# Kernel optimization log

Hardware: AMD Instinct MI355X
Metric: run time of the kernel (lower is better)

## Reference

```python
import jax, jax.numpy as jnp
import numpy as np
from jax import lax

B, N, F, H = 8, 2048, 256, 128
RATIO = 0.5
NUM_LAYERS = 2
K = int(N * RATIO) + 1  # num coarse nodes per layer


def setup_inputs() -> dict:
    key = jax.random.key(0)
    ks = jax.random.split(key, 8)
    x = jax.random.normal(ks[0], (B, N, F), dtype=jnp.float32)
    a = jax.random.uniform(ks[1], (B, N, N), dtype=jnp.float32)
    adj = (a < 0.005).astype(jnp.float32)
    adj = jnp.maximum(adj, adj.transpose(0, 2, 1))
    mask = jnp.ones((B, N), dtype=jnp.float32)
    W1 = jax.random.normal(ks[2], (F, H), dtype=jnp.float32) * (1.0 / np.sqrt(F))
    b1 = jnp.zeros((H,), dtype=jnp.float32)
    Watt = jax.random.normal(ks[3], (H, 1), dtype=jnp.float32) * (1.0 / np.sqrt(H))
    batt = jnp.zeros((1,), dtype=jnp.float32)
    W2 = jax.random.normal(ks[4], (H, F), dtype=jnp.float32) * (1.0 / np.sqrt(H))
    b2 = jnp.zeros((F,), dtype=jnp.float32)
    return {"x": x, "adj": adj, "mask": mask, "W1": W1, "b1": b1,
            "Watt": Watt, "batt": batt, "W2": W2, "b2": b2}


def dense_gcn(x, adj, W, b, mask):
    # PyG DenseGCNConv with add_loop=True: set diag to 1, sym-normalize, propagate
    n = adj.shape[-1]
    eye = jnp.eye(n, dtype=adj.dtype)
    a = adj * (1.0 - eye) + eye
    d = jnp.maximum(a.sum(-1), 1.0) ** -0.5            # [B,N]
    an = d[..., :, None] * a * d[..., None, :]
    out = jnp.einsum('bnm,bmh->bnh', an, x @ W) + b
    return out * mask[..., None]


def normalize_batch_adj(adj):
    n = adj.shape[-1]
    A = adj + jnp.eye(n, dtype=adj.dtype)
    d = jnp.maximum(A.sum(-1), 1.0) ** -0.5
    newA = d[..., :, None] * A * d[..., None, :]
    row_nonzero = (adj.sum(-1) > 0).astype(adj.dtype)  # zero out isolated-node rows
    return row_nonzero[..., None] * newA


def coarsen_block(x, adj, Watt, batt, k):
    norm_adj = normalize_batch_adj(adj)
    # attention GCN -> squared -> sigmoid
    alpha = jnp.einsum('bnm,bm->bn', norm_adj, (x @ Watt + batt).squeeze(-1))
    alpha = jax.nn.sigmoid(alpha ** 2)                 # [B,N]
    topv, topi = lax.top_k(alpha, k)
    cut = topv[:, -1]                                  # k-th largest value per graph
    cut_alpha = jax.nn.relu(alpha + 1e-7 - cut[:, None])
    S = norm_adj * cut_alpha[:, None, :]               # scale columns
    S = S / jnp.maximum(jnp.abs(S).sum(-1, keepdims=True), 1e-12)  # L1 row-normalize
    x2 = jnp.einsum('bnm,bnf->bmf', S, x)              # S^T x
    A2 = jnp.einsum('bnm,bnk,bkl->bml', S, adj, S)     # S^T A S
    A2 = jnp.floor(A2 * 1e4) / 1e4                     # 4-digit floor quantization
    return x2, A2, S, topi


def reference(x, adj, mask, W1, b1, Watt, batt, W2, b2):
    x1 = jax.nn.relu(dense_gcn(x, adj, W1, b1, mask))  # [B,N,H]
    coarse_x, new_adj = x1, adj
    for _ in range(NUM_LAYERS):
        coarse_x, new_adj, S, topi = coarsen_block(coarse_x, new_adj, Watt, batt, K)
    x2 = dense_gcn(coarse_x, new_adj, W2, b2, mask)    # [B,N,F]
    # JumpingKnowledge 'cat' of pooled readouts
    return jnp.concatenate([x1.mean(axis=1), x2.mean(axis=1)], axis=-1)  # [B,H+F]
```

## Files before the change

### kernel.cpp

```cpp
#include <hip/hip_runtime.h>
#include <math.h>

#define NN 2048
#define NB 8
#define FF 256
#define HH 128
#define KSEL 1025
#define NROWS (NB*NN)
#define MPAD 1152
#define MC (MPAD*NB)
#define LMAX 64
#define MI 6
#define RSTRIDE 2052
#define ZIDX 2048
#define LP 72

typedef unsigned short ushort_t;
typedef __attribute__((ext_vector_type(8))) short short8;
typedef __attribute__((ext_vector_type(4))) float f32x4;

__device__ inline ushort_t f2bf(float f) {
  unsigned u = __float_as_uint(f);
  unsigned r = (u + 0x7FFFu + ((u >> 16) & 1u)) >> 16;
  return (ushort_t)r;
}
__device__ inline float bf2f(ushort_t u) {
  unsigned x = ((unsigned)u) << 16;
  return __uint_as_float(x);
}

#define GLDS16(g, l) __builtin_amdgcn_global_load_lds( \
    (const __attribute__((address_space(1))) unsigned int*)(g), \
    (__attribute__((address_space(3))) unsigned int*)(l), 16, 0, 0)

__global__ __launch_bounds__(256) void rowstats_k(const float* __restrict__ A,
                                                  ushort_t* __restrict__ klist,
                                                  int* __restrict__ kcnt,
                                                  float* __restrict__ diag,
                                                  float* __restrict__ dgcn,
                                                  float* __restrict__ dnorm,
                                                  float* __restrict__ rz, int R) {
  int gw = (blockIdx.x * 256 + threadIdx.x) >> 6;
  int lane = threadIdx.x & 63;
  int b = gw / R, i = gw - b * R;
  const float4* row = (const float4*)(A + (long long)gw * R);
  int R4 = R >> 2;
  float s = 0.f;
  ushort_t* lst = klist ? (klist + (long long)gw * LMAX) : (ushort_t*)0;
  int base = 0;
  for (int j = lane; j < R4; j += 64) {
    float4 v = row[j];
    s += v.x + v.y + v.z + v.w;
    if (klist) {
      int c0 = (v.x != 0.f), c1 = (v.y != 0.f), c2 = (v.z != 0.f), c3 = (v.w != 0.f);
      int c = c0 + c1 + c2 + c3;
      int pref = c;
#pragma unroll
      for (int off = 1; off < 64; off <<= 1) {
        int t = __shfl_up(pref, off);
        if (lane >= off) pref += t;
      }
      int tot = __shfl(pref, 63);
      int p = base + pref - c;
      int col = j * 4;
      if (c0) { if (p < LMAX) lst[p] = (ushort_t)col;       p++; }
      if (c1) { if (p < LMAX) lst[p] = (ushort_t)(col + 1); p++; }
      if (c2) { if (p < LMAX) lst[p] = (ushort_t)(col + 2); p++; }
      if (c3) { if (p < LMAX) lst[p] = (ushort_t)(col + 3); p++; }
      base += tot;
    }
  }
  for (int off = 32; off > 0; off >>= 1) s += __shfl_down(s, off);
  if (lane == 0) {
    float dg = A[(long long)gw * R + i];
    diag[gw] = dg;
    dgcn[gw]  = rsqrtf(fmaxf(s - dg + 1.f, 1.f));
    dnorm[gw] = rsqrtf(fmaxf(s + 1.f, 1.f));
    rz[gw]    = s > 0.f ? 1.f : 0.f;
    if (kcnt) kcnt[gw] = base < LMAX ? base : LMAX;
  }
}

__global__ __launch_bounds__(256) void rowstatsw_k(const float* __restrict__ A,
                                                   const float* __restrict__ X,
                                                   const float* __restrict__ Watt,
                                                   const float* __restrict__ batt,
                                                   float* __restrict__ dnorm,
                                                   float* __restrict__ rz,
                                                   float* __restrict__ w, int R) {
  int gw = (blockIdx.x * 256 + threadIdx.x) >> 6;
  int lane = threadIdx.x & 63;
  int b = gw / R;
  const float4* row = (const float4*)(A + (long long)gw * R);
  int R4 = R >> 2;
  float s = 0.f;
  for (int j = lane; j < R4; j += 64) {
    float4 v = row[j];
    s += v.x + v.y + v.z + v.w;
  }
  for (int off = 32; off > 0; off >>= 1) s += __shfl_xor(s, off);
  float dn = rsqrtf(fmaxf(s + 1.f, 1.f));
  const float* xr = X + (long long)gw * HH;
  float t = xr[lane] * Watt[lane] + xr[lane + 64] * Watt[lane + 64];
  for (int off = 32; off > 0; off >>= 1) t += __shfl_down(t, off);
  if (lane == 0) {
    dnorm[gw] = dn;
    rz[gw]    = s > 0.f ? 1.f : 0.f;
    w[gw] = dn * (t + batt[0]);
  }
}

__global__ __launch_bounds__(256) void spmm1e_k(const ushort_t* __restrict__ klist,
                                                const int* __restrict__ kcnt,
                                                const float* __restrict__ dgcn,
                                                const float* __restrict__ diag,
                                                const float* __restrict__ b1,
                                                const float* __restrict__ mask,
                                                const float* __restrict__ Watt,
                                                const float* __restrict__ batt,
                                                const float* __restrict__ dnorm,
                                                const float* __restrict__ xw,
                                                float* __restrict__ xa,
                                                float* __restrict__ w) {
  int bid = blockIdx.x;
  int sw = (bid & 7) * ((int)gridDim.x >> 3) + (bid >> 3);
  int gw = (sw * 256 + threadIdx.x) >> 6;
  int lane = threadIdx.x & 63;
  int b = gw >> 11;
  int cnt = kcnt[gw];
  const ushort_t* kl = klist + (long long)gw * LMAX;
  int myk = (lane < cnt) ? (int)kl[lane] : 0;
  float myd = dgcn[b * NN + myk];
  float s0 = 0.f, s1 = 0.f;
  for (int t = 0; t < cnt; t++) {
    int k = __shfl(myk, t);
    float d = __shfl(myd, t);
    const float* xr = xw + ((long long)b * NN + k) * HH;
    s0 += d * xr[lane];
    s1 += d * xr[lane + 64];
  }
  long long o = (long long)gw * HH;
  float d = dgcn[gw];
  float dgv = diag[gw];
  float mv = mask[gw];
  float xw0 = xw[o + lane], xw1v = xw[o + lane + 64];
  float t0 = d * (s0 + (1.f - dgv) * d * xw0) + b1[lane];
  float t1 = d * (s1 + (1.f - dgv) * d * xw1v) + b1[lane + 64];
  t0 *= mv; t1 *= mv;
  float x0 = fmaxf(t0, 0.f), x1 = fmaxf(t1, 0.f);
  xa[o + lane] = x0;
  xa[o + lane + 64] = x1;
  float t = x0 * Watt[lane] + x1 * Watt[lane + 64];
  for (int off = 32; off > 0; off >>= 1) t += __shfl_down(t, off);
  if (lane == 0) w[gw] = dnorm[gw] * (t + batt[0]);
}

__global__ __launch_bounds__(256) void spmm2_k(const ushort_t* __restrict__ klistC,
                                               const int* __restrict__ kcntC,
                                               const float* __restrict__ scalev,
                                               const float* __restrict__ cwk,
                                               const float* __restrict__ xa,
                                               float* __restrict__ x2c) {
  int bid = blockIdx.x;
  int sw = (bid & 7) * ((int)gridDim.x >> 3) + (bid >> 3);
  int gw = (sw * 256 + threadIdx.x) >> 6;
  int lane = threadIdx.x & 63;
  int b = gw / MPAD;
  int cnt = kcntC[gw];
  const ushort_t* kl = klistC + (long long)gw * LP;
  int c64 = cnt < 64 ? cnt : 64;
  int myk = (lane < c64) ? (int)kl[lane] : 0;
  float myc = scalev[b * NN + myk];
  float s0 = 0.f, s1 = 0.f;
  for (int t = 0; t < c64; t++) {
    int k = __shfl(myk, t);
    float c = __shfl(myc, t);
    const float* xr = xa + ((long long)b * NN + k) * HH;
    s0 += c * xr[lane];
    s1 += c * xr[lane + 64];
  }
  if (cnt > 64) {
    int k = kl[64];
    float c = scalev[b * NN + k];
    const float* xr = xa + ((long long)b * NN + k) * HH;
    s0 += c * xr[lane];
    s1 += c * xr[lane + 64];
  }
  float cw = cwk[gw];
  long long o = (long long)gw * HH;
  x2c[o + lane] = cw * s0;
  x2c[o + lane + 64] = cw * s1;
}

__global__ __launch_bounds__(256) void alphaL_k(const ushort_t* __restrict__ klist,
                                                const int* __restrict__ kcnt,
                                                const float* __restrict__ w,
                                                const float* __restrict__ dnorm,
                                                const float* __restrict__ rz,
                                                float* __restrict__ alpha) {
  int gw = (blockIdx.x * 256 + threadIdx.x) >> 6;
  int lane = threadIdx.x & 63;
  int b = gw >> 11, i = gw & (NN - 1);
  int cnt = kcnt[gw];
  float s = 0.f;
  if (lane < cnt) s = w[(long long)b * NN + klist[(long long)gw * LMAX + lane]];
  for (int off = 32; off > 0; off >>= 1) s += __shfl_down(s, off);
  if (lane == 0) {
    float aa = rz[gw] * dnorm[gw] * (s + w[(long long)b * NN + i]);
    aa = aa * aa;
    alpha[(long long)b * NN + i] = 1.f / (1.f + expf(-aa));
  }
}

__global__ __launch_bounds__(256) void alpha_k(const float* __restrict__ A,
                                               const float* __restrict__ w,
                                               const float* __restrict__ dnorm,
                                               const float* __restrict__ rz,
                                               float* __restrict__ alpha, int R) {
  int gw = (blockIdx.x * 256 + threadIdx.x) >> 6;
  int lane = threadIdx.x & 63;
  int b = gw / R, i = gw - b * R;
  const float4* row = (const float4*)(A + (long long)gw * R);
  const float4* wb4 = (const float4*)(w + (long long)b * R);
  int R4 = R >> 2;
  float s = 0.f;
  for (int j = lane; j < R4; j += 64) {
    float4 a = row[j], ww = wb4[j];
    s += a.x * ww.x + a.y * ww.y + a.z * ww.z + a.w * ww.w;
  }
  for (int off = 32; off > 0; off >>= 1) s += __shfl_down(s, off);
  if (lane == 0) {
    float aa = rz[gw] * dnorm[gw] * (s + w[(long long)b * R + i]);
    aa = aa * aa;
    alpha[(long long)b * NN + i] = 1.f / (1.f + expf(-aa));
  }
}

__global__ __launch_bounds__(1024) void topkeep_k(const float* __restrict__ alpha,
                                                  const float* __restrict__ dnorm,
                                                  const float* __restrict__ rz,
                                                  float* __restrict__ colw,
                                                  int* __restrict__ keepidx) {
  __shared__ unsigned vals[NN];
  __shared__ int hist[256];
  __shared__ int wsum[32];
  __shared__ unsigned selp_s;
  __shared__ int selr_s;
  int b = blockIdx.x, t = threadIdx.x;
  vals[t] = __float_as_uint(alpha[b * NN + t]);
  vals[t + 1024] = __float_as_uint(alpha[b * NN + t + 1024]);
  if (t == 0) { selp_s = 0u; selr_s = KSEL; }
  __syncthreads();
  for (int shift = 24; shift >= 0; shift -= 8) {
    if (t < 256) hist[t] = 0;
    __syncthreads();
    unsigned pre = selp_s; int rank = selr_s;
    unsigned hm = (shift == 24) ? 0u : (0xFFFFFFFFu << (shift + 8));
    for (int e = t; e < NN; e += 1024) {
      unsigned v = vals[e];
      if ((v & hm) == (pre & hm)) atomicAdd(&hist[(v >> shift) & 255], 1);
    }
    __syncthreads();
    for (int off2 = 1; off2 < 256; off2 <<= 1) {
      int v = 0;
      if (t < 256 - off2) v = hist[t + off2];
      __syncthreads();
      if (t < 256 - off2) hist[t] += v;
      __syncthreads();
    }
    if (t < 256) {
      int cge = hist[t];
      int cgt = (t == 255) ? 0 : hist[t + 1];
      if (cge >= rank && cgt < rank) {
        selp_s = pre | ((unsigned)t << shift);
        selr_s = rank - cgt;
      }
    }
    __syncthreads();
  }
  float cu = __uint_as_float(selp_s);
  float a0 = __uint_as_float(vals[t]);
  float a1 = __uint_as_float(vals[t + 1024]);
  float c0 = dnorm[b * NN + t]        * fmaxf(a0 + 1e-7f - cu, 0.f);
  float c1 = dnorm[b * NN + t + 1024] * fmaxf(a1 + 1e-7f - cu, 0.f);
  colw[b * NN + t] = c0;
  colw[b * NN + t + 1024] = c1;
  int f0 = (c0 != 0.f && rz[b * NN + t]        != 0.f) ? 1 : 0;
  int f1 = (c1 != 0.f && rz[b * NN + t + 1024] != 0.f) ? 1 : 0;
  int lane = t & 63, wid = t >> 6;
  unsigned long long m0 = __ballot(f0);
  unsigned long long m1 = __ballot(f1);
  if (lane == 0) { wsum[wid] = __popcll(m0); wsum[16 + wid] = __popcll(m1); }
  __syncthreads();
  if (t == 0) { int run = 0; for (int i2 = 0; i2 < 32; i2++) { int v = wsum[i2]; wsum[i2] = run; run += v; } }
  __syncthreads();
  unsigned long long lm = (1ull << lane) - 1ull;
  int p0 = wsum[wid] + __popcll(m0 & lm);
  int p1 = wsum[16 + wid] + __popcll(m1 & lm);
  if (t < MPAD) keepidx[b * MPAD + t] = -1;
  if (t + 1024 < MPAD) keepidx[b * MPAD + t + 1024] = -1;
  __syncthreads();
  if (f0 && p0 < MPAD) keepidx[b * MPAD + p0] = t;
  if (f1 && p1 < MPAD) keepidx[b * MPAD + p1] = t + 1024;
}

__global__ __launch_bounds__(1024) void topcolw_k(const float* __restrict__ alpha,
                                                  const float* __restrict__ dnorm,
                                                  float* __restrict__ colw) {
  __shared__ unsigned vals[NN];
  __shared__ int hist[256];
  __shared__ unsigned selp_s;
  __shared__ int selr_s;
  int b = blockIdx.x, t = threadIdx.x;
  vals[t] = __float_as_uint(alpha[b * NN + t]);
  vals[t + 1024] = (t + 1024 >= MPAD) ? __float_as_uint(0.5f)
                                      : __float_as_uint(alpha[b * NN + t + 1024]);
  if (t == 0) { selp_s = 0u; selr_s = KSEL; }
  __syncthreads();
  for (int shift = 24; shift >= 0; shift -= 8) {
    if (t < 256) hist[t] = 0;
    __syncthreads();
    unsigned pre = selp_s; int rank = selr_s;
    unsigned hm = (shift == 24) ? 0u : (0xFFFFFFFFu << (shift + 8));
    for (int e = t; e < NN; e += 1024) {
      unsigned v = vals[e];
      if ((v & hm) == (pre & hm)) atomicAdd(&hist[(v >> shift) & 255], 1);
    }
    __syncthreads();
    for (int off2 = 1; off2 < 256; off2 <<= 1) {
      int v = 0;
      if (t < 256 - off2) v = hist[t + off2];
      __syncthreads();
      if (t < 256 - off2) hist[t] += v;
      __syncthreads();
    }
    if (t < 256) {
      int cge = hist[t];
      int cgt = (t == 255) ? 0 : hist[t + 1];
      if (cge >= rank && cgt < rank) {
        selp_s = pre | ((unsigned)t << shift);
        selr_s = rank - cgt;
      }
    }
    __syncthreads();
  }
  float cu = __uint_as_float(selp_s);
  for (int ii = t; ii < MPAD; ii += 1024) {
    float c = fmaxf(__uint_as_float(vals[ii]) + 1e-7f - cu, 0.f);
    colw[b * MPAD + ii] = dnorm[b * MPAD + ii] * c;
  }
}

__global__ __launch_bounds__(256) void scaleL_k(const ushort_t* __restrict__ klist,
                                                const int* __restrict__ kcnt,
                                                const float* __restrict__ colw,
                                                const float* __restrict__ dnorm,
                                                const float* __restrict__ rz,
                                                float* __restrict__ scale) {
  int gw = (blockIdx.x * 256 + threadIdx.x) >> 6;
  int lane = threadIdx.x & 63;
  int b = gw >> 11, i = gw & (NN - 1);
  int cnt = kcnt[gw];
  float s = 0.f;
  if (lane < cnt) s = colw[(long long)b * NN + klist[(long long)gw * LMAX + lane]];
  for (int off = 32; off > 0; off >>= 1) s += __shfl_down(s, off);
  if (lane == 0) {
    float rsum = rz[gw] * dnorm[gw] * (s + colw[(long long)b * NN + i]);
    scale[gw] = rz[gw] * dnorm[gw] / fmaxf(rsum, 1e-12f);
  }
}

__global__ __launch_bounds__(256) void scale_k(const float* __restrict__ A,
                                               const float* __restrict__ colw,
                                               const float* __restrict__ dnorm,
                                               const float* __restrict__ rz,
                                               float* __restrict__ scale, int R) {
  int gw = (blockIdx.x * 256 + threadIdx.x) >> 6;
  int lane = threadIdx.x & 63;
  int b = gw / R, i = gw - b * R;
  const float4* row = (const float4*)(A + (long long)gw * R);
  const float4* cw4 = (const float4*)(colw + (long long)b * R);
  int R4 = R >> 2;
  float s = 0.f;
  for (int j = lane; j < R4; j += 64) {
    float4 a = row[j], c = cw4[j];
    s += a.x * c.x + a.y * c.y + a.z * c.z + a.w * c.w;
  }
  for (int off = 32; off > 0; off >>= 1) s += __shfl_down(s, off);
  if (lane == 0) {
    float rsum = rz[gw] * dnorm[gw] * (s + colw[(long long)b * R + i]);
    scale[gw] = rz[gw] * dnorm[gw] / fmaxf(rsum, 1e-12f);
  }
}

__global__ __launch_bounds__(256) void packlist_k(const ushort_t* __restrict__ klist,
                                                  const int* __restrict__ kcnt,
                                                  const int* __restrict__ keepidx,
                                                  const float* __restrict__ colw,
                                                  ushort_t* __restrict__ klistC,
                                                  int* __restrict__ kcntC,
                                                  float* __restrict__ cwk) {
  int g = blockIdx.x * 256 + threadIdx.x;
  int b = g / MPAD;
  int rj = keepidx[g];
  ushort_t* dst = klistC + (long long)g * LP;
  int cnt = 0;
  if (rj >= 0) {
    long long gr = (long long)b * NN + rj;
    int c = kcnt[gr];
    const ushort_t* src = klist + gr * LMAX;
    for (int t = 0; t < c; t++) dst[t] = src[t];
    dst[c] = (ushort_t)rj;
    cnt = c + 1;
  }
  kcntC[g] = cnt;
  cwk[g] = (rj >= 0) ? colw[b * NN + rj] : 0.f;
  int pad = (cnt + 7) & ~7;
  for (int t = cnt; t < pad; t++) dst[t] = (ushort_t)ZIDX;
}

__global__ void zero_k(float* __restrict__ p) {
  p[blockIdx.x * 256 + threadIdx.x] = 0.f;
}

__global__ __launch_bounds__(256) void sparseA2f_k(const ushort_t* __restrict__ klist,
                                                   const int* __restrict__ kcnt,
                                                   const int* __restrict__ keepidx,
                                                   const float* __restrict__ scalev,
                                                   const ushort_t* __restrict__ klistC,
                                                   const int* __restrict__ kcntC,
                                                   const float* __restrict__ cwk,
                                                   float* __restrict__ A2cF,
                                                   ushort_t* __restrict__ A2cH,
                                                   ushort_t* __restrict__ A2cL) {
  __shared__ float Rs[3 * RSTRIDE * 2];
  int i0 = blockIdx.x * MI;
  int b = i0 / MPAD, im0 = i0 - b * MPAD;
  int tid = threadIdx.x;
  int wid = tid >> 6, lane = tid & 63;
  const float* sb = scalev + (long long)b * NN;

  float4 z4 = make_float4(0.f, 0.f, 0.f, 0.f);
  for (int n = tid * 4; n < 3 * RSTRIDE * 2; n += 1024) *(float4*)&Rs[n] = z4;
  __syncthreads();

  for (int rr = wid; rr < MI; rr += 4) {
    int r = keepidx[i0 + rr];
    if (r < 0) continue;
    int p = rr >> 1, q = rr & 1;
    float* plane = Rs + p * RSTRIDE * 2;
    long long gr = (long long)b * NN + r;
    int cr = kcnt[gr];
    int myk = (lane < cr) ? (int)klist[gr * LMAX + lane] : r;
    float mycoef = sb[myk];
    int mycnt = kcnt[(long long)b * NN + myk];
    for (int i = 0; i < cr; i++) {
      int k = __shfl(myk, i);
      float coef = __shfl(mycoef, i);
      int ck = __shfl(mycnt, i);
      if (lane < ck) {
        int n = (int)klist[((long long)b * NN + k) * LMAX + lane];
        plane[n * 2 + q] += coef;
      }
    }
    float coef = sb[r];
    if (lane < cr) plane[myk * 2 + q] += coef;
  }
  __syncthreads();

  for (int c = tid; c < NN; c += 256) {
    float sc = sb[c];
#pragma unroll
    for (int p = 0; p < 3; p++) {
      float2* e = (float2*)&Rs[(p * RSTRIDE + c) * 2];
      float2 v = *e; v.x *= sc; v.y *= sc; *e = v;
    }
  }
  __syncthreads();

  float cwi[MI];
#pragma unroll
  for (int r = 0; r < MI; r++) cwi[r] = cwk[i0 + r];
  long long ob = (long long)b * MPAD * MPAD + (long long)im0 * MPAD;
  for (int j = tid; j < MPAD; j += 256) {
    int cnt = kcntC[b * MPAD + j];
    const ushort_t* kl = klistC + (long long)(b * MPAD + j) * LP;
    float sx0 = 0.f, sy0 = 0.f, sx1 = 0.f, sy1 = 0.f, sx2 = 0.f, sy2 = 0.f;
    int rounds = (cnt + 7) >> 3;
    for (int t0 = 0; t0 < rounds; t0++) {
      uint4 kv = *(const uint4*)(kl + t0 * 8);
      const ushort_t* kp = (const ushort_t*)&kv;
#pragma unroll
      for (int t = 0; t < 8; t++) {
        int c = kp[t];
        float2 v0 = *(const float2*)&Rs[(0 * RSTRIDE + c) * 2];
        float2 v1 = *(const float2*)&Rs[(1 * RSTRIDE + c) * 2];
        float2 v2 = *(const float2*)&Rs[(2 * RSTRIDE + c) * 2];
        sx0 += v0.x; sy0 += v0.y;
        sx1 += v1.x; sy1 += v1.y;
        sx2 += v2.x; sy2 += v2.y;
      }
    }
    float sv[MI] = {sx0, sy0, sx1, sy1, sx2, sy2};
    float cwj = cwk[b * MPAD + j];
#pragma unroll
    for (int r = 0; r < MI; r++) {
      float vq = floorf(cwi[r] * cwj * sv[r] * 10000.f) / 10000.f;
      ushort_t h = f2bf(vq);
      long long o = ob + (long long)r * MPAD + j;
      A2cF[o] = vq;
      A2cH[o] = h;
      A2cL[o] = f2bf(vq - bf2f(h));
    }
  }
}

__global__ void writeS2c_k(const float* __restrict__ A2c, const float* __restrict__ scale,
                           const float* __restrict__ colw,
                           ushort_t* __restrict__ Sh, ushort_t* __restrict__ Sl) {
  int g = blockIdx.x * 256 + threadIdx.x;
  int bl = g / (MPAD / 4);
  int k = (g - bl * (MPAD / 4)) * 4;
  int b = bl / MPAD, l = bl - b * MPAD;
  long long o = (long long)bl * MPAD + k;
  float cw = colw[b * MPAD + l];
  float4 sc = *(const float4*)(scale + b * MPAD + k);
  float4 av = *(const float4*)(A2c + o);
  float v0 = sc.x * (av.x + (float)(k     == l)) * cw;
  float v1 = sc.y * (av.y + (float)(k + 1 == l)) * cw;
  float v2 = sc.z * (av.z + (float)(k + 2 == l)) * cw;
  float v3 = sc.w * (av.w + (float)(k + 3 == l)) * cw;
  ushort_t h0 = f2bf(v0), h1 = f2bf(v1), h2 = f2bf(v2), h3 = f2bf(v3);
  *(uint2*)&Sh[o] = make_uint2((unsigned)h0 | ((unsigned)h1 << 16),
                               (unsigned)h2 | ((unsigned)h3 << 16));
  ushort_t l0 = f2bf(v0 - bf2f(h0)), l1 = f2bf(v1 - bf2f(h1));
  ushort_t l2 = f2bf(v2 - bf2f(h2)), l3 = f2bf(v3 - bf2f(h3));
  *(uint2*)&Sl[o] = make_uint2((unsigned)l0 | ((unsigned)l1 << 16),
                               (unsigned)l2 | ((unsigned)l3 << 16));
}

template<int SA, int SB, int EPI, int BN>
__global__ __launch_bounds__(256) void mgemm_k(
    const ushort_t* __restrict__ Ah, const ushort_t* __restrict__ Al,
    const ushort_t* __restrict__ Bh, const ushort_t* __restrict__ Bl,
    float* __restrict__ Co, ushort_t* __restrict__ Toh, ushort_t* __restrict__ Tol,
    float* __restrict__ rs, float* __restrict__ dgv,
    int M, int Ncol, int K, long long sA, long long sB, long long sC,
    int gx, int ks, long long sPart) {
  constexpr int NJ = BN / 32;
  __shared__ ushort_t Ahs[128 * 32];
  __shared__ ushort_t Bhs[BN * 32];
  __shared__ ushort_t Als[SA ? 128 * 32 : 64];
  __shared__ ushort_t Bls[SB ? BN * 32 : 64];

  int tid = threadIdx.x;
  int id = blockIdx.x;
  long long bz = id & 7;
  int rest = id >> 3;
  int kslice = rest % ks;
  int t0 = rest / ks;
  int tn = t0 % gx, tm = t0 / gx;
  int n0 = tn * BN, m0 = tm * 128;
  const ushort_t* Ahb = Ah + bz * sA;
  const ushort_t* Alb = SA ? (Al + bz * sA) : Ah;
  const ushort_t* Bhb = Bh + bz * sB;
  const ushort_t* Blb = SB ? (Bl + bz * sB) : Bh;

  int sr = tid >> 2;
  int sc = (tid & 3) * 8;
  int lane = tid & 63, w = tid >> 6;
  int wm = (w >> 1) * 64, wn = (w & 1) * (BN / 2);
  int fr = lane & 15;
  int fo = (lane >> 4) * 8;
  int q = lane >> 4;

  f32x4 acc[4][NJ];
  f32x4 zz = {0.f, 0.f, 0.f, 0.f};
#pragma unroll
  for (int i = 0; i < 4; i++)
#pragma unroll
    for (int j = 0; j < NJ; j++) acc[i][j] = zz;

  int Kpc = K / ks;
  int kbeg = kslice * Kpc;
  for (int k0 = kbeg; k0 < kbeg + Kpc; k0 += 32) {
    __syncthreads();
#pragma unroll
    for (int r = 0; r < 128; r += 64) {
      GLDS16(Ahb + (long long)(m0 + sr + r) * K + k0 + sc, &Ahs[(r + sr) * 32 + sc]);
      if constexpr (SA) {
        GLDS16(Alb + (long long)(m0 + sr + r) * K + k0 + sc, &Als[(r + sr) * 32 + sc]);
      }
    }
#pragma unroll
    for (int r = 0; r < BN; r += 64) {
      GLDS16(Bhb + (long long)(n0 + sr + r) * K + k0 + sc, &Bhs[(r + sr) * 32 + sc]);
      if constexpr (SB) {
        GLDS16(Blb + (long long)(n0 + sr + r) * K + k0 + sc, &Bls[(r + sr) * 32 + sc]);
      }
    }
    __syncthreads();

    short8 ah[4], al[4], bh[NJ], bl[NJ];
#pragma unroll
    for (int i = 0; i < 4; i++) {
      ah[i] = *(const short8*)&Ahs[(wm + i * 16 + fr) * 32 + fo];
      if constexpr (SA) al[i] = *(const short8*)&Als[(wm + i * 16 + fr) * 32 + fo];
    }
#pragma unroll
    for (int j = 0; j < NJ; j++) {
      bh[j] = *(const short8*)&Bhs[(wn + j * 16 + fr) * 32 + fo];
      if constexpr (SB) bl[j] = *(const short8*)&Bls[(wn + j * 16 + fr) * 32 + fo];
    }
#pragma unroll
    for (int i = 0; i < 4; i++)
#pragma unroll
      for (int j = 0; j < NJ; j++) {
        acc[i][j] = __builtin_amdgcn_mfma_f32_16x16x32_bf16(ah[i], bh[j], acc[i][j], 0, 0, 0);
        if constexpr (SB)
          acc[i][j] = __builtin_amdgcn_mfma_f32_16x16x32_bf16(ah[i], bl[j], acc[i][j], 0, 0, 0);
        if constexpr (SA)
          acc[i][j] = __builtin_amdgcn_mfma_f32_16x16x32_bf16(al[i], bh[j], acc[i][j], 0, 0, 0);
      }
  }

  if constexpr (EPI == 6) {
#pragma unroll
    for (int i = 0; i < 4; i++)
#pragma unroll
      for (int r = 0; r < 4; r++) {
        int row = m0 + wm + i * 16 + q * 4 + r;
        long long rb = bz * sC + (long long)row * Ncol;
        float rp = 0.f;
#pragma unroll
        for (int j = 0; j < NJ; j++) {
          int col = n0 + wn + j * 16 + fr;
          float vq = floorf(acc[i][j][r] * 10000.f) / 10000.f;
          Co[rb + col] = vq;
          rp += vq;
          if (col == row) dgv[bz * MPAD + row] = vq;
        }
#pragma unroll
        for (int o2 = 8; o2 > 0; o2 >>= 1) rp += __shfl_down(rp, o2, 16);
        if (fr == 0) atomicAdd(&rs[bz * MPAD + row], rp);
      }
  } else {
#pragma unroll
    for (int i = 0; i < 4; i++)
#pragma unroll
      for (int j = 0; j < NJ; j++)
#pragma unroll
        for (int r = 0; r < 4; r++) {
          float v = acc[i][j][r];
          int row = m0 + wm + i * 16 + q * 4 + r;
          int col = n0 + wn + j * 16 + fr;
          long long idx = bz * sC + (long long)row * Ncol + col;
          if constexpr (EPI == 0) {
            Co[kslice * sPart + idx] = v;
          } else {
            ushort_t h = f2bf(v);
            Toh[idx] = h;
            Tol[idx] = f2bf(v - bf2f(h));
          }
        }
  }
}

__global__ void dstat_k(const float* __restrict__ rs, const float* __restrict__ dgv,
                        float* __restrict__ dgcn) {
  int g = blockIdx.x * 256 + threadIdx.x;
  dgcn[g] = rsqrtf(fmaxf(rs[g] - dgv[g] + 1.f, 1.f));
}

__global__ __launch_bounds__(256) void wfin_k(const float* __restrict__ A3,
                                              const float* __restrict__ dgcn,
                                              const float* __restrict__ diag,
                                              float* __restrict__ wv) {
  int gw = (blockIdx.x * 256 + threadIdx.x) >> 6;
  int lane = threadIdx.x & 63;
  int b = gw / MPAD;
  const float4* row = (const float4*)(A3 + (long long)gw * MPAD);
  const float4* d4 = (const float4*)(dgcn + (long long)b * MPAD);
  float s = 0.f;
  for (int j = lane; j < MPAD / 4; j += 64) {
    float4 a = row[j], d = d4[j];
    s += a.x * d.x + a.y * d.y + a.z * d.z + a.w * d.w;
  }
  for (int off = 32; off > 0; off >>= 1) s += __shfl_down(s, off);
  if (lane == 0) {
    float dl = dgcn[gw];
    wv[gw] = dl * (s - dl * diag[gw] + dl);
  }
}

__global__ __launch_bounds__(256) void zfin_k(const float* __restrict__ A2c,
                                              const float* __restrict__ scalev,
                                              const float* __restrict__ colwv,
                                              const float* __restrict__ wv,
                                              float* __restrict__ zv) {
  int gw = (blockIdx.x * 256 + threadIdx.x) >> 6;
  int lane = threadIdx.x & 63;
  int b = gw / MPAD;
  const float4* row = (const float4*)(A2c + (long long)gw * MPAD);
  const float4* c4 = (const float4*)(colwv + (long long)b * MPAD);
  const float4* w4 = (const float4*)(wv + (long long)b * MPAD);
  float s = 0.f;
  for (int j = lane; j < MPAD / 4; j += 64) {
    float4 a = row[j], c = c4[j], w = w4[j];
    s += a.x * c.x * w.x + a.y * c.y * w.y + a.z * c.z * w.z + a.w * c.w * w.w;
  }
  for (int off = 32; off > 0; off >>= 1) s += __shfl_down(s, off);
  if (lane == 0) {
    zv[gw] = scalev[gw] * (s + colwv[gw] * wv[gw]);
  }
}

__global__ void zx_k(const float* __restrict__ zv, const float* __restrict__ x2c,
                     float* __restrict__ part) {
  int b = blockIdx.y, c = blockIdx.x, h = threadIdx.x;
  const float* p = x2c + ((long long)(b * MPAD + c * 128)) * HH + h;
  const float* zp = zv + b * MPAD + c * 128;
  float s = 0.f;
  for (int r = 0; r < 128; r++) s += zp[r] * p[(long long)r * HH];
  part[(b * 9 + c) * HH + h] = s;
}

__global__ __launch_bounds__(256) void fout2_k(const float* __restrict__ part,
                                               const float* __restrict__ W2,
                                               const float* __restrict__ b2,
                                               float* __restrict__ out) {
  __shared__ float wx3[HH];
  int b = blockIdx.x, f = threadIdx.x;
  if (f < HH) {
    float s = 0.f;
    for (int c = 0; c < 9; c++) s += part[(b * 9 + c) * HH + f];
    wx3[f] = s;
  }
  __syncthreads();
  float s = 0.f;
  for (int h = 0; h < HH; h++) s += wx3[h] * W2[h * FF + f];
  out[b * (HH + FF) + HH + f] = b2[f] + s * (1.f / NN);
}

__global__ void pmean_k(const float* __restrict__ X, float* __restrict__ part,
                        int Nn, int Fd, int rpc) {
  int b = blockIdx.y, c = blockIdx.x, f = threadIdx.x;
  const float* p = X + ((long long)b * Nn + (long long)c * rpc) * Fd + f;
  float s = 0.f;
  for (int r = 0; r < rpc; r++) s += p[(long long)r * Fd];
  part[((long long)b * gridDim.x + c) * Fd + f] = s;
}

__global__ void fmean_k(const float* __restrict__ part, int nch, int Fd, float corr,
                        const float* __restrict__ bias, float* __restrict__ out, int outoff) {
  int b = blockIdx.x, f = threadIdx.x;
  float s = 0.f;
  for (int c = 0; c < nch; c++) s += part[((long long)b * nch + c) * Fd + f];
  float cv = bias ? corr * bias[f] : 0.f;
  out[b * (HH + FF) + outoff + f] = s * (1.f / NN) + cv;
}

__global__ __launch_bounds__(256) void gemm_k(const float* __restrict__ A, const float* __restrict__ B,
                                              float* __restrict__ C,
                                              int M, int Nw, int Kk,
                                              long long sA, long long sB, long long sC) {
  __shared__ float As[16][128];
  __shared__ float Bs[16][128];
  int tid = threadIdx.x;
  int n0 = blockIdx.x * 128, m0 = blockIdx.y * 128;
  int bz = blockIdx.z;
  const float* Ab = A + (long long)bz * sA;
  const float* Bb = B + (long long)bz * sB;
  float* Cb = C + (long long)bz * sC;
  float acc[8][8];
#pragma unroll
  for (int i = 0; i < 8; i++)
#pragma unroll
    for (int j = 0; j < 8; j++) acc[i][j] = 0.f;
  int tx = tid & 15, ty = tid >> 4;

  for (int k0 = 0; k0 < Kk; k0 += 16) {
    {
      int r = tid >> 2, c = (tid & 3) << 2;
#pragma unroll
      for (int rr = 0; rr < 2; rr++) {
        int rrow = r + rr * 64;
        float4 v = *(const float4*)(Ab + (long long)(m0 + rrow) * Kk + k0 + c);
        As[c + 0][rrow] = v.x; As[c + 1][rrow] = v.y;
        As[c + 2][rrow] = v.z; As[c + 3][rrow] = v.w;
      }
    }
    {
      int kk = tid >> 5, cc = (tid & 31) << 2;
#pragma unroll
      for (int k2 = 0; k2 < 2; k2++) {
        float4 v = *(const float4*)(Bb + (long long)(k0 + kk + k2 * 8) * Nw + n0 + cc);
        *(float4*)&Bs[kk + k2 * 8][cc] = v;
      }
    }
    __syncthreads();
#pragma unroll
    for (int kk = 0; kk < 16; kk++) {
      float a[8], bb[8];
      *(float4*)&a[0]  = *(float4*)&As[kk][ty * 8];
      *(float4*)&a[4]  = *(float4*)&As[kk][ty * 8 + 4];
      *(float4*)&bb[0] = *(float4*)&Bs[kk][tx * 8];
      *(float4*)&bb[4] = *(float4*)&Bs[kk][tx * 8 + 4];
#pragma unroll
      for (int i = 0; i < 8; i++)
#pragma unroll
        for (int j = 0; j < 8; j++) acc[i][j] += a[i] * bb[j];
    }
    __syncthreads();
  }
#pragma unroll
  for (int i = 0; i < 8; i++) {
    float* cp = Cb + (long long)(m0 + ty * 8 + i) * Nw + n0 + tx * 8;
    *(float4*)cp = *(float4*)&acc[i][0];
    *(float4*)(cp + 4) = *(float4*)&acc[i][4];
  }
}

extern "C" void kernel_launch(void* const* d_in, const int* in_sizes, int n_in,
                              void* d_out, int out_size, void* d_ws, size_t ws_size,
                              hipStream_t stream) {
  const float* x    = (const float*)d_in[0];
  const float* adj  = (const float*)d_in[1];
  const float* mask = (const float*)d_in[2];
  const float* W1   = (const float*)d_in[3];
  const float* b1   = (const float*)d_in[4];
  const float* Watt = (const float*)d_in[5];
  const float* batt = (const float*)d_in[6];
  const float* W2   = (const float*)d_in[7];
  const float* b2   = (const float*)d_in[8];
  float* out = (float*)d_out;

  const long long CSTR = (long long)MPAD * NN;
  const long long CTOT = (long long)NB * CSTR;
  const long long M2   = (long long)MPAD * MPAD;
  const long long M2T  = (long long)NB * M2;
  const long long NH   = (long long)NROWS * HH;
  const long long MH   = (long long)MC * HH;

  float* ws = (float*)d_ws;
  long long off = 0;
  ushort_t* S2cH = (ushort_t*)(ws + off); off += M2T;
  float* A2CR = ws + off; off += M2T * 2;
  float* TcF  = ws + off; off += CTOT;
  float* A3F  = ws + off; off += CTOT / 2;
  float* xa   = ws + off; off += NH;
  float* x2c  = ws + off; off += MH;
  float* x3c  = ws + off; off += MH;
  float* diag   = ws + off; off += NROWS;
  float* dgcn   = ws + off; off += NROWS;
  float* dnorm  = ws + off; off += NROWS;
  float* rz     = ws + off; off += NROWS;
  float* wv     = ws + off; off += NROWS;
  float* alphav = ws + off; off += (long long)NB * NN;
  float* colwv  = ws + off; off += NROWS;
  float* scalev = ws + off; off += NROWS;
  off += NROWS / 2;
  off += NROWS / 2;
  int* keepidx  = (int*)(ws + off); off += NB * MPAD;
  float* cwk    = ws + off; off += MC;
  float* partm  = ws + off; off += NB * 16 * FF;

  ushort_t* S2cL = S2cH + M2T;
  float* A2cF = A2CR;
  ushort_t* A2cH = (ushort_t*)(A2CR + M2T);
  ushort_t* A2cL = A2cH + M2T;

  ushort_t* klist = (ushort_t*)x3c;
  int* kcnt = (int*)(x3c + (long long)NROWS * (LMAX / 2));
  ushort_t* klistC = (ushort_t*)(x3c + (long long)NROWS * (LMAX / 2) + NROWS);
  int* kcntC = (int*)(x3c + (long long)NROWS * (LMAX / 2) + NROWS + (long long)MC * LP / 2);

  float* u1 = TcF;
  ushort_t* Tc2H = (ushort_t*)TcF;
  ushort_t* Tc2L = Tc2H + M2T;

  float* rsum = alphav;

  rowstats_k<<<NROWS / 4, 256, 0, stream>>>(adj, klist, kcnt, diag, dgcn, dnorm, rz, NN);
  gemm_k<<<dim3(1, NN / 128, NB), 256, 0, stream>>>(
      x, W1, u1, NN, HH, FF,
      (long long)NN * FF, 0, (long long)NN * HH);
  spmm1e_k<<<NROWS / 4, 256, 0, stream>>>(klist, kcnt, dgcn, diag, b1, mask,
                                          Watt, batt, dnorm, u1, xa, wv);
  pmean_k<<<dim3(16, NB), HH, 0, stream>>>(xa, partm, NN, HH, 128);
  fmean_k<<<NB, HH, 0, stream>>>(partm, 16, HH, 0.f, 0, out, 0);

  alphaL_k<<<NROWS / 4, 256, 0, stream>>>(klist, kcnt, wv, dnorm, rz, alphav);
  topkeep_k<<<NB, 1024, 0, stream>>>(alphav, dnorm, rz, colwv, keepidx);
  scaleL_k<<<NROWS / 4, 256, 0, stream>>>(klist, kcnt, colwv, dnorm, rz, scalev);
  packlist_k<<<MC / 256, 256, 0, stream>>>(klist, kcnt, keepidx, colwv, klistC, kcntC, cwk);
  sparseA2f_k<<<MC / MI, 256, 0, stream>>>(klist, kcnt, keepidx, scalev,
                                           klistC, kcntC, cwk, A2cF, A2cH, A2cL);
  spmm2_k<<<MC / 4, 256, 0, stream>>>(klistC, kcntC, scalev, cwk, xa, x2c);

  rowstatsw_k<<<MC / 4, 256, 0, stream>>>(A2cF, x2c, Watt, batt, dnorm, rz, wv, MPAD);
  alpha_k<<<MC / 4, 256, 0, stream>>>(A2cF, wv, dnorm, rz, alphav, MPAD);
  topcolw_k<<<NB, 1024, 0, stream>>>(alphav, dnorm, colwv);
  scale_k<<<MC / 4, 256, 0, stream>>>(A2cF, colwv, dnorm, rz, scalev, MPAD);
  writeS2c_k<<<(int)(M2T / 4 / 256), 256, 0, stream>>>(A2cF, scalev, colwv, S2cH, S2cL);
  mgemm_k<1, 1, 1, 64><<<(MPAD / 128) * (MPAD / 64) * NB, 256, 0, stream>>>(
      S2cH, S2cL, A2cH, A2cL, 0, Tc2H, Tc2L, 0, 0,
      MPAD, MPAD, MPAD, M2, M2, M2, MPAD / 64, 1, 0);
  zero_k<<<MC / 256, 256, 0, stream>>>(rsum);
  mgemm_k<1, 1, 6, 64><<<(MPAD / 128) * (MPAD / 64) * NB, 256, 0, stream>>>(
      S2cH, S2cL, Tc2H, Tc2L, A3F, 0, 0, rsum, diag,
      MPAD, MPAD, MPAD, M2, M2, M2, MPAD / 64, 1, 0);

  dstat_k<<<MC / 256, 256, 0, stream>>>(rsum, diag, dgcn);
  wfin_k<<<MC / 4, 256, 0, stream>>>(A3F, dgcn, diag, wv);
  zfin_k<<<MC / 4, 256, 0, stream>>>(A2cF, scalev, colwv, wv, alphav );
  zx_k<<<dim3(9, NB), HH, 0, stream>>>(alphav, x2c, partm);
  fout2_k<<<NB, FF, 0, stream>>>(partm, W2, b2, out);
}
```

Measured before the change: 694.2 us.

## Exploit symmetry of S^T A S to compute only lower-triangle tiles

The second product S^T (A S) is symmetric, so the GEMM now launches only the lower-triangular tile set (90 of 162 tiles per batch) and mirrors each off-diagonal result into the transposed position. The fused row-sum/diagonal atomics epilogue and the zero/dstat kernels are removed; degree statistics are instead recomputed by reusing rowstats_k on the quantized A3 matrix. This roughly halves the MFMA work of that GEMM, at the cost of strided transposed stores and an extra full pass over A3 to get row sums. Mirroring assumes bitwise symmetry of the computed product, which may not hold exactly in floating point with floor quantization.

```diff
diff --git a/kernel.cpp b/kernel.cpp
--- a/kernel.cpp
+++ b/kernel.cpp
@@ -419,10 +419,6 @@
   for (int t = cnt; t < pad; t++) dst[t] = (ushort_t)ZIDX;
 }
 
-__global__ void zero_k(float* __restrict__ p) {
-  p[blockIdx.x * 256 + threadIdx.x] = 0.f;
-}
-
 __global__ __launch_bounds__(256) void sparseA2f_k(const ushort_t* __restrict__ klist,
                                                    const int* __restrict__ kcnt,
                                                    const int* __restrict__ keepidx,
@@ -539,12 +535,11 @@
                                (unsigned)l2 | ((unsigned)l3 << 16));
 }
 
-template<int SA, int SB, int EPI, int BN>
+template<int SA, int SB, int EPI, int BN, int SYMM>
 __global__ __launch_bounds__(256) void mgemm_k(
     const ushort_t* __restrict__ Ah, const ushort_t* __restrict__ Al,
     const ushort_t* __restrict__ Bh, const ushort_t* __restrict__ Bl,
     float* __restrict__ Co, ushort_t* __restrict__ Toh, ushort_t* __restrict__ Tol,
-    float* __restrict__ rs, float* __restrict__ dgv,
     int M, int Ncol, int K, long long sA, long long sB, long long sC,
     int gx, int ks, long long sPart) {
   constexpr int NJ = BN / 32;
@@ -559,7 +554,14 @@
   int rest = id >> 3;
   int kslice = rest % ks;
   int t0 = rest / ks;
-  int tn = t0 % gx, tm = t0 / gx;
+  int tm, tn;
+  if constexpr (SYMM) {
+    tm = 0;
+    while ((tm + 1) * (tm + 2) <= t0) tm++;
+    tn = t0 - tm * (tm + 1);
+  } else {
+    tn = t0 % gx; tm = t0 / gx;
+  }
   int n0 = tn * BN, m0 = tm * 128;
   const ushort_t* Ahb = Ah + bz * sA;
   const ushort_t* Alb = SA ? (Al + bz * sA) : Ah;
@@ -624,52 +626,30 @@
       }
   }
 
-  if constexpr (EPI == 6) {
-#pragma unroll
-    for (int i = 0; i < 4; i++)
+#pragma unroll
+  for (int i = 0; i < 4; i++)
+#pragma unroll
+    for (int j = 0; j < NJ; j++)
 #pragma unroll
       for (int r = 0; r < 4; r++) {
+        float v = acc[i][j][r];
         int row = m0 + wm + i * 16 + q * 4 + r;
-        long long rb = bz * sC + (long long)row * Ncol;
-        float rp = 0.f;
-#pragma unroll
-        for (int j = 0; j < NJ; j++) {
-          int col = n0 + wn + j * 16 + fr;
-          float vq = floorf(acc[i][j][r] * 10000.f) / 10000.f;
-          Co[rb + col] = vq;
-          rp += vq;
-          if (col == row) dgv[bz * MPAD + row] = vq;
-        }
-#pragma unroll
-        for (int o2 = 8; o2 > 0; o2 >>= 1) rp += __shfl_down(rp, o2, 16);
-        if (fr == 0) atomicAdd(&rs[bz * MPAD + row], rp);
-      }
-  } else {
-#pragma unroll
-    for (int i = 0; i < 4; i++)
-#pragma unroll
-      for (int j = 0; j < NJ; j++)
-#pragma unroll
-        for (int r = 0; r < 4; r++) {
-          float v = acc[i][j][r];
-          int row = m0 + wm + i * 16 + q * 4 + r;
-          int col = n0 + wn + j * 16 + fr;
-          long long idx = bz * sC + (long long)row * Ncol + col;
-          if constexpr (EPI == 0) {
-            Co[kslice * sPart + idx] = v;
-          } else {
-            ushort_t h = f2bf(v);
-            Toh[idx] = h;
-            Tol[idx] = f2bf(v - bf2f(h));
+        int col = n0 + wn + j * 16 + fr;
+        long long idx = bz * sC + (long long)row * Ncol + col;
+        if constexpr (EPI == 0) {
+          Co[kslice * sPart + idx] = v;
+        } else if constexpr (EPI == 1) {
+          ushort_t h = f2bf(v);
+          Toh[idx] = h;
+          Tol[idx] = f2bf(v - bf2f(h));
+        } else {
+          float vq = floorf(v * 10000.f) / 10000.f;
+          Co[idx] = vq;
+          if constexpr (SYMM) {
+            if (tn < 2 * tm) Co[bz * sC + (long long)col * Ncol + row] = vq;
           }
         }
-  }
-}
-
-__global__ void dstat_k(const float* __restrict__ rs, const float* __restrict__ dgv,
-                        float* __restrict__ dgcn) {
-  int g = blockIdx.x * 256 + threadIdx.x;
-  dgcn[g] = rsqrtf(fmaxf(rs[g] - dgv[g] + 1.f, 1.f));
+      }
 }
 
 __global__ __launch_bounds__(256) void wfin_k(const float* __restrict__ A3,
@@ -879,8 +859,6 @@
   ushort_t* Tc2H = (ushort_t*)TcF;
   ushort_t* Tc2L = Tc2H + M2T;
 
-  float* rsum = alphav;
-
   rowstats_k<<<NROWS / 4, 256, 0, stream>>>(adj, klist, kcnt, diag, dgcn, dnorm, rz, NN);
   gemm_k<<<dim3(1, NN / 128, NB), 256, 0, stream>>>(
       x, W1, u1, NN, HH, FF,
@@ -903,15 +881,14 @@
   topcolw_k<<<NB, 1024, 0, stream>>>(alphav, dnorm, colwv);
   scale_k<<<MC / 4, 256, 0, stream>>>(A2cF, colwv, dnorm, rz, scalev, MPAD);
   writeS2c_k<<<(int)(M2T / 4 / 256), 256, 0, stream>>>(A2cF, scalev, colwv, S2cH, S2cL);
-  mgemm_k<1, 1, 1, 64><<<(MPAD / 128) * (MPAD / 64) * NB, 256, 0, stream>>>(
-      S2cH, S2cL, A2cH, A2cL, 0, Tc2H, Tc2L, 0, 0,
+  mgemm_k<1, 1, 1, 64, 0><<<(MPAD / 128) * (MPAD / 64) * NB, 256, 0, stream>>>(
+      S2cH, S2cL, A2cH, A2cL, 0, Tc2H, Tc2L,
       MPAD, MPAD, MPAD, M2, M2, M2, MPAD / 64, 1, 0);
-  zero_k<<<MC / 256, 256, 0, stream>>>(rsum);
-  mgemm_k<1, 1, 6, 64><<<(MPAD / 128) * (MPAD / 64) * NB, 256, 0, stream>>>(
-      S2cH, S2cL, Tc2H, Tc2L, A3F, 0, 0, rsum, diag,
-      MPAD, MPAD, MPAD, M2, M2, M2, MPAD / 64, 1, 0);
-
-  dstat_k<<<MC / 256, 256, 0, stream>>>(rsum, diag, dgcn);
+  mgemm_k<1, 1, 6, 64, 1><<<90 * NB, 256, 0, stream>>>(
+      S2cH, S2cL, Tc2H, Tc2L, A3F, 0, 0,
+      MPAD, MPAD, MPAD, M2, M2, M2, 0, 1, 0);
+
+  rowstats_k<<<MC / 4, 256, 0, stream>>>(A3F, 0, 0, diag, dgcn, dnorm, rz, MPAD);
   wfin_k<<<MC / 4, 256, 0, stream>>>(A3F, dgcn, diag, wv);
   zfin_k<<<MC / 4, 256, 0, stream>>>(A2cF, scalev, colwv, wv, alphav );
   zx_k<<<dim3(9, NB), HH, 0, stream>>>(alphav, x2c, partm);
```

Result: faster. 660.9 us (-4.8%).
